# Kernel optimization log

Measured on AMD Instinct MI355X. Metric: run time of the kernel, lower is better.

The kernel has to match this reference:

```python
import jax, jax.numpy as jnp
import numpy as np

RADIUS = 0.08          # fixed search radius (module init arg)
MAX_NEIGHBORS = 64     # pad cap; expected ~35 neighbors/query at this density


def setup_inputs() -> dict:
    key = jax.random.key(0)
    k1, k2 = jax.random.split(key)
    return {
        "inp_positions": jax.random.uniform(k1, (16384, 3), dtype=jnp.float32),
        "out_positions": jax.random.uniform(k2, (16384, 3), dtype=jnp.float32),
    }


def reference(inp_positions, out_positions):
    """Fixed-radius neighbor search.

    Returns (neighbors_index [M, MAX_NEIGHBORS] int32, padded with -1,
             neighbors_row_splits [M+1] int32) --- the padded/static-shape
    equivalent of the ragged CSR output of NeighborSearchReturn.
    """
    r2 = jnp.float32(RADIUS * RADIUS)
    # pairwise squared distances [M, N]
    diff = out_positions[:, None, :] - inp_positions[None, :, :]
    d2 = jnp.sum(diff * diff, axis=-1)
    within = d2 <= r2                                   # [M, N] bool
    counts = jnp.minimum(within.sum(axis=1), MAX_NEIGHBORS).astype(jnp.int32)
    # rank in-radius points first (nearest first); -inf for out-of-radius
    score = jnp.where(within, -d2, -jnp.inf)
    _, idx = jax.lax.top_k(score, MAX_NEIGHBORS)        # [M, K]
    valid = jnp.arange(MAX_NEIGHBORS, dtype=jnp.int32)[None, :] < counts[:, None]
    neighbors_index = jnp.where(valid, idx, -1).astype(jnp.int32)
    row_splits = jnp.concatenate(
        [jnp.zeros((1,), jnp.int32), jnp.cumsum(counts).astype(jnp.int32)]
    )
    return neighbors_index, row_splits
```

## Files before the change

### kernel.cpp

```cpp
#include <hip/hip_runtime.h>

#define MAXNB 64
#define CAP   128
#define GRID  12
#define NCELL (GRID * GRID * GRID)

__device__ __forceinline__ int cell_of(float x, float y, float z) {
  int cx = min(GRID - 1, max(0, (int)(x * (float)GRID)));
  int cy = min(GRID - 1, max(0, (int)(y * (float)GRID)));
  int cz = min(GRID - 1, max(0, (int)(z * (float)GRID)));
  return (cz * GRID + cy) * GRID + cx;
}

__global__ __launch_bounds__(256) void build_kernel(
    const float* __restrict__ inp, const float* __restrict__ qry,
    float4* __restrict__ qpack, int* __restrict__ pcell, int* __restrict__ ppos,
    int* __restrict__ pcellcnt, int n, int m) {
  int i = blockIdx.x * 256 + threadIdx.x;
  if (i < n) {
    float x = inp[3 * i], y = inp[3 * i + 1], z = inp[3 * i + 2];
    int c = cell_of(x, y, z);
    pcell[i] = c;
    ppos[i] = atomicAdd(&pcellcnt[c], 1);
  }
  if (i < m) {
    qpack[i] = make_float4(qry[3 * i], qry[3 * i + 1], qry[3 * i + 2], 0.f);
  }
}

__global__ __launch_bounds__(256) void cellscan_kernel(
    const int* __restrict__ pcnt, int* __restrict__ pstart) {
  __shared__ int part[256];
  int t = threadIdx.x;
  int base = t * 7;
  int v[7];
  int s = 0;
#pragma unroll
  for (int i = 0; i < 7; ++i) {
    int idx = base + i;
    int c = (idx < NCELL) ? pcnt[idx] : 0;
    v[i] = c;
    s += c;
  }
  part[t] = s;
  __syncthreads();
  for (int off = 1; off < 256; off <<= 1) {
    int vv = (t >= off) ? part[t - off] : 0;
    __syncthreads();
    part[t] += vv;
    __syncthreads();
  }
  int run = (t == 0) ? 0 : part[t - 1];
#pragma unroll
  for (int i = 0; i < 7; ++i) {
    int idx = base + i;
    if (idx <= NCELL) pstart[idx] = run;
    run += v[i];
  }
}

__global__ __launch_bounds__(256) void scatter_kernel(
    const float* __restrict__ inp, const int* __restrict__ pcell,
    const int* __restrict__ ppos, const int* __restrict__ pstart,
    float4* __restrict__ psorted, int n) {
  int i = blockIdx.x * 256 + threadIdx.x;
  if (i < n) {
    float4 p = make_float4(inp[3 * i], inp[3 * i + 1], inp[3 * i + 2],
                           __int_as_float(i));
    psorted[pstart[pcell[i]] + ppos[i]] = p;
  }
}

__global__ __launch_bounds__(256) void scanrank_kernel(
    const float4* __restrict__ psorted, const float4* __restrict__ qpack,
    const int* __restrict__ pstart, int* __restrict__ cnt,
    int* __restrict__ nbr) {
#pragma clang fp contract(off)
  const float R2 = (float)(0.08 * 0.08);
  const float RM = 0.0801f;
  __shared__ unsigned long long skey[4][CAP];
  __shared__ int srk0[4][10];
  __shared__ int sracc[4][10];
  __shared__ int souts[4][MAXNB];
  int w = threadIdx.x >> 6;
  int lane = threadIdx.x & 63;
  int q = blockIdx.x * 4 + w;
  float4 Q = qpack[q];

  int x0 = max(0, (int)floorf((Q.x - RM) * (float)GRID));
  int x1 = min(GRID - 1, (int)floorf((Q.x + RM) * (float)GRID));
  int y0 = max(0, (int)floorf((Q.y - RM) * (float)GRID));
  int y1 = min(GRID - 1, (int)floorf((Q.y + RM) * (float)GRID));
  int z0 = max(0, (int)floorf((Q.z - RM) * (float)GRID));
  int z1 = min(GRID - 1, (int)floorf((Q.z + RM) * (float)GRID));

  int nr = 0, tot = 0;
  for (int z = z0; z <= z1; ++z) {
    for (int y = y0; y <= y1; ++y) {
      int rb = (z * GRID + y) * GRID;
      int k0 = pstart[rb + x0];
      int k1 = pstart[rb + x1 + 1];
      if (lane == 0) { srk0[w][nr] = k0; sracc[w][nr] = tot; }
      tot += k1 - k0;
      ++nr;
    }
  }

  int nc = 0;
  for (int tb = 0; tb < tot; tb += 64) {
    int t = tb + lane;
    bool hit = false;
    float d2 = 0.f;
    int id = 0;
    if (t < tot) {
      int r = 0;
#pragma unroll
      for (int s = 1; s < 9; ++s)
        if (s < nr && t >= sracc[w][s]) r = s;
      int k = srk0[w][r] + (t - sracc[w][r]);
      float4 P = psorted[k];
      float dx = Q.x - P.x;
      float dy = Q.y - P.y;
      float dz = Q.z - P.z;
      d2 = dx * dx + dy * dy + dz * dz;
      id = __float_as_int(P.w);
      hit = d2 <= R2;
    }
    unsigned long long b = __ballot(hit);
    int pre = __builtin_amdgcn_mbcnt_hi(
        (unsigned)(b >> 32), __builtin_amdgcn_mbcnt_lo((unsigned)b, 0));
    int slot = nc + pre;
    if (hit && slot < CAP) {
      skey[w][slot] =
          ((unsigned long long)(unsigned)__float_as_int(d2) << 32) |
          (unsigned)id;
    }
    nc += __popcll(b);
  }

  if (lane == 0) cnt[q] = nc;
  souts[w][lane] = -1;

  int ncc = nc < CAP ? nc : CAP;
  for (int c = lane; c < ncc; c += 64) {
    unsigned long long mykey = skey[w][c];
    int rank = 0;
    for (int j = 0; j < ncc; ++j)
      rank += (skey[w][j] < mykey);
    if (rank < MAXNB) souts[w][rank] = (int)(unsigned)mykey;
  }

  nbr[(size_t)q * MAXNB + lane] = souts[w][lane];
}

__global__ __launch_bounds__(256) void splits_kernel(
    const int* __restrict__ cnt, int* __restrict__ rs, int m) {
  __shared__ int part[256];
  int t = threadIdx.x;
  int per = m / 256;
  int base = t * per;
  const int4* c4 = (const int4*)(cnt + base);
  int s = 0;
#pragma unroll
  for (int i = 0; i < 16; ++i) {
    int4 v = c4[i];
    s += min(v.x, MAXNB) + min(v.y, MAXNB) + min(v.z, MAXNB) + min(v.w, MAXNB);
  }
  part[t] = s;
  __syncthreads();
  for (int off = 1; off < 256; off <<= 1) {
    int v = (t >= off) ? part[t - off] : 0;
    __syncthreads();
    part[t] += v;
    __syncthreads();
  }
  int run = (t == 0) ? 0 : part[t - 1];
  if (t == 0) rs[0] = 0;
#pragma unroll
  for (int i = 0; i < 16; ++i) {
    int4 v = c4[i];
    run += min(v.x, MAXNB); rs[base + 4 * i + 1] = run;
    run += min(v.y, MAXNB); rs[base + 4 * i + 2] = run;
    run += min(v.z, MAXNB); rs[base + 4 * i + 3] = run;
    run += min(v.w, MAXNB); rs[base + 4 * i + 4] = run;
  }
}

extern "C" void kernel_launch(void* const* d_in, const int* in_sizes, int n_in,
                              void* d_out, int out_size, void* d_ws, size_t ws_size,
                              hipStream_t stream) {
  const float* inp = (const float*)d_in[0];
  const float* qry = (const float*)d_in[1];
  int n = in_sizes[0] / 3;
  int m = in_sizes[1] / 3;

  char* ws = (char*)d_ws;
  size_t off = 0;
  float4* qpack   = (float4*)(ws + off); off += (size_t)m * 16;
  float4* psorted = (float4*)(ws + off); off += (size_t)n * 16;
  int* pcell    = (int*)(ws + off); off += (size_t)n * 4;
  int* ppos     = (int*)(ws + off); off += (size_t)n * 4;
  int* cnt      = (int*)(ws + off); off += (size_t)m * 4;
  int* pcellcnt = (int*)(ws + off); off += (size_t)NCELL * 4;
  int* pstart   = (int*)(ws + off); off += (size_t)(NCELL + 1) * 4;

  int* nbr = (int*)d_out;
  int* rs = nbr + (size_t)m * MAXNB;

  hipMemsetAsync(pcellcnt, 0, (size_t)NCELL * 4, stream);

  int mx = n > m ? n : m;
  hipLaunchKernelGGL(build_kernel, dim3((mx + 255) / 256), dim3(256), 0, stream,
                     inp, qry, qpack, pcell, ppos, pcellcnt, n, m);
  hipLaunchKernelGGL(cellscan_kernel, dim3(1), dim3(256), 0, stream,
                     pcellcnt, pstart);
  hipLaunchKernelGGL(scatter_kernel, dim3((n + 255) / 256), dim3(256), 0, stream,
                     inp, pcell, ppos, pstart, psorted, n);
  hipLaunchKernelGGL(scanrank_kernel, dim3(m / 4), dim3(256), 0, stream,
                     psorted, qpack, pstart, cnt, nbr);
  hipLaunchKernelGGL(splits_kernel, dim3(1), dim3(256), 0, stream, cnt, rs, m);
}
```

Before: 93.00 us.

## Fuse cell scan and row-split scan into last-block tails of preceding kernels

Removes the two single-block scan kernels by having the last block to finish build_kernel and scanrank_kernel, detected through an atomic done counter, perform the cell prefix scan and the row_splits scan. The scatter kernel now recomputes cell indices and takes slot positions from a second atomic counter array, so pcell/ppos are no longer stored. This cuts two kernel launches and some global traffic, at the cost of a serialized tail in the last block and atomic loads in the scans. The in-cell order of points now depends on atomic scheduling, but distance-based ranking keeps the output the same.

```diff
diff --git a/kernel.cpp b/kernel.cpp
--- a/kernel.cpp
+++ b/kernel.cpp
@@ -14,32 +14,39 @@
 
 __global__ __launch_bounds__(256) void build_kernel(
     const float* __restrict__ inp, const float* __restrict__ qry,
-    float4* __restrict__ qpack, int* __restrict__ pcell, int* __restrict__ ppos,
-    int* __restrict__ pcellcnt, int n, int m) {
+    float4* __restrict__ qpack, int* __restrict__ pcellcnt,
+    int* __restrict__ pstart, int* __restrict__ done, int n, int m) {
   int i = blockIdx.x * 256 + threadIdx.x;
   if (i < n) {
     float x = inp[3 * i], y = inp[3 * i + 1], z = inp[3 * i + 2];
-    int c = cell_of(x, y, z);
-    pcell[i] = c;
-    ppos[i] = atomicAdd(&pcellcnt[c], 1);
+    atomicAdd(&pcellcnt[cell_of(x, y, z)], 1);
   }
   if (i < m) {
     qpack[i] = make_float4(qry[3 * i], qry[3 * i + 1], qry[3 * i + 2], 0.f);
   }
-}
-
-__global__ __launch_bounds__(256) void cellscan_kernel(
-    const int* __restrict__ pcnt, int* __restrict__ pstart) {
+  __syncthreads();
+  __shared__ int lastf;
+  if (threadIdx.x == 0) {
+    int t = __hip_atomic_fetch_add(done, 1, __ATOMIC_ACQ_REL,
+                                   __HIP_MEMORY_SCOPE_AGENT);
+    lastf = (t == (int)gridDim.x - 1);
+  }
+  __syncthreads();
+  if (!lastf) return;
+
   __shared__ int part[256];
   int t = threadIdx.x;
   int base = t * 7;
   int v[7];
   int s = 0;
 #pragma unroll
-  for (int i = 0; i < 7; ++i) {
-    int idx = base + i;
-    int c = (idx < NCELL) ? pcnt[idx] : 0;
-    v[i] = c;
+  for (int k = 0; k < 7; ++k) {
+    int idx = base + k;
+    int c = (idx < NCELL)
+                ? __hip_atomic_load(&pcellcnt[idx], __ATOMIC_RELAXED,
+                                    __HIP_MEMORY_SCOPE_AGENT)
+                : 0;
+    v[k] = c;
     s += c;
   }
   part[t] = s;
@@ -52,29 +59,30 @@
   }
   int run = (t == 0) ? 0 : part[t - 1];
 #pragma unroll
-  for (int i = 0; i < 7; ++i) {
-    int idx = base + i;
+  for (int k = 0; k < 7; ++k) {
+    int idx = base + k;
     if (idx <= NCELL) pstart[idx] = run;
-    run += v[i];
+    run += v[k];
   }
 }
 
 __global__ __launch_bounds__(256) void scatter_kernel(
-    const float* __restrict__ inp, const int* __restrict__ pcell,
-    const int* __restrict__ ppos, const int* __restrict__ pstart,
-    float4* __restrict__ psorted, int n) {
+    const float* __restrict__ inp, const int* __restrict__ pstart,
+    int* __restrict__ pcellcnt2, float4* __restrict__ psorted, int n) {
   int i = blockIdx.x * 256 + threadIdx.x;
   if (i < n) {
-    float4 p = make_float4(inp[3 * i], inp[3 * i + 1], inp[3 * i + 2],
-                           __int_as_float(i));
-    psorted[pstart[pcell[i]] + ppos[i]] = p;
+    float x = inp[3 * i], y = inp[3 * i + 1], z = inp[3 * i + 2];
+    int c = cell_of(x, y, z);
+    int pos = atomicAdd(&pcellcnt2[c], 1);
+    psorted[pstart[c] + pos] = make_float4(x, y, z, __int_as_float(i));
   }
 }
 
 __global__ __launch_bounds__(256) void scanrank_kernel(
     const float4* __restrict__ psorted, const float4* __restrict__ qpack,
     const int* __restrict__ pstart, int* __restrict__ cnt,
-    int* __restrict__ nbr) {
+    int* __restrict__ nbr, int* __restrict__ rs, int* __restrict__ done,
+    int m) {
 #pragma clang fp contract(off)
   const float R2 = (float)(0.08 * 0.08);
   const float RM = 0.0801f;
@@ -138,7 +146,9 @@
     nc += __popcll(b);
   }
 
-  if (lane == 0) cnt[q] = nc;
+  if (lane == 0)
+    __hip_atomic_store(&cnt[q], nc, __ATOMIC_RELAXED,
+                       __HIP_MEMORY_SCOPE_AGENT);
   souts[w][lane] = -1;
 
   int ncc = nc < CAP ? nc : CAP;
@@ -151,20 +161,26 @@
   }
 
   nbr[(size_t)q * MAXNB + lane] = souts[w][lane];
-}
-
-__global__ __launch_bounds__(256) void splits_kernel(
-    const int* __restrict__ cnt, int* __restrict__ rs, int m) {
+
+  __syncthreads();
+  __shared__ int lastf;
+  if (threadIdx.x == 0) {
+    int t = __hip_atomic_fetch_add(done, 1, __ATOMIC_ACQ_REL,
+                                   __HIP_MEMORY_SCOPE_AGENT);
+    lastf = (t == (int)gridDim.x - 1);
+  }
+  __syncthreads();
+  if (!lastf) return;
+
   __shared__ int part[256];
   int t = threadIdx.x;
   int per = m / 256;
   int base = t * per;
-  const int4* c4 = (const int4*)(cnt + base);
   int s = 0;
-#pragma unroll
-  for (int i = 0; i < 16; ++i) {
-    int4 v = c4[i];
-    s += min(v.x, MAXNB) + min(v.y, MAXNB) + min(v.z, MAXNB) + min(v.w, MAXNB);
+  for (int i = 0; i < per; ++i) {
+    int c = __hip_atomic_load(&cnt[base + i], __ATOMIC_RELAXED,
+                              __HIP_MEMORY_SCOPE_AGENT);
+    s += min(c, MAXNB);
   }
   part[t] = s;
   __syncthreads();
@@ -176,13 +192,11 @@
   }
   int run = (t == 0) ? 0 : part[t - 1];
   if (t == 0) rs[0] = 0;
-#pragma unroll
-  for (int i = 0; i < 16; ++i) {
-    int4 v = c4[i];
-    run += min(v.x, MAXNB); rs[base + 4 * i + 1] = run;
-    run += min(v.y, MAXNB); rs[base + 4 * i + 2] = run;
-    run += min(v.z, MAXNB); rs[base + 4 * i + 3] = run;
-    run += min(v.w, MAXNB); rs[base + 4 * i + 4] = run;
+  for (int i = 0; i < per; ++i) {
+    int c = __hip_atomic_load(&cnt[base + i], __ATOMIC_RELAXED,
+                              __HIP_MEMORY_SCOPE_AGENT);
+    run += min(c, MAXNB);
+    rs[base + i + 1] = run;
   }
 }
 
@@ -198,25 +212,22 @@
   size_t off = 0;
   float4* qpack   = (float4*)(ws + off); off += (size_t)m * 16;
   float4* psorted = (float4*)(ws + off); off += (size_t)n * 16;
-  int* pcell    = (int*)(ws + off); off += (size_t)n * 4;
-  int* ppos     = (int*)(ws + off); off += (size_t)n * 4;
   int* cnt      = (int*)(ws + off); off += (size_t)m * 4;
-  int* pcellcnt = (int*)(ws + off); off += (size_t)NCELL * 4;
-  int* pstart   = (int*)(ws + off); off += (size_t)(NCELL + 1) * 4;
+  int* pcellcnt  = (int*)(ws + off); off += (size_t)NCELL * 4;
+  int* pcellcnt2 = (int*)(ws + off); off += (size_t)NCELL * 4;
+  int* done      = (int*)(ws + off); off += 2 * 4;
+  int* pstart    = (int*)(ws + off); off += (size_t)(NCELL + 1) * 4;
 
   int* nbr = (int*)d_out;
   int* rs = nbr + (size_t)m * MAXNB;
 
-  hipMemsetAsync(pcellcnt, 0, (size_t)NCELL * 4, stream);
+  hipMemsetAsync(pcellcnt, 0, (size_t)(2 * NCELL + 2) * 4, stream);
 
   int mx = n > m ? n : m;
   hipLaunchKernelGGL(build_kernel, dim3((mx + 255) / 256), dim3(256), 0, stream,
-                     inp, qry, qpack, pcell, ppos, pcellcnt, n, m);
-  hipLaunchKernelGGL(cellscan_kernel, dim3(1), dim3(256), 0, stream,
-                     pcellcnt, pstart);
+                     inp, qry, qpack, pcellcnt, pstart, &done[0], n, m);
   hipLaunchKernelGGL(scatter_kernel, dim3((n + 255) / 256), dim3(256), 0, stream,
-                     inp, pcell, ppos, pstart, psorted, n);
+                     inp, pstart, pcellcnt2, psorted, n);
   hipLaunchKernelGGL(scanrank_kernel, dim3(m / 4), dim3(256), 0, stream,
-                     psorted, qpack, pstart, cnt, nbr);
-  hipLaunchKernelGGL(splits_kernel, dim3(1), dim3(256), 0, stream, cnt, rs, m);
-}
+                     psorted, qpack, pstart, cnt, nbr, rs, &done[1], m);
+}
```

Result: slower. 209.5 us (+125.3%).
